# Performance work log

Hardware: AMD Instinct MI355X
Metric: run time of the kernel (lower is better)

The kernel has to match this reference:

```python
import jax, jax.numpy as jnp
import numpy as np

B, N, F = 16, 4096, 3

def setup_inputs() -> dict:
    key = jax.random.key(0)
    k1, k2 = jax.random.split(key)
    array1 = jax.random.normal(k1, (B, N, F), dtype=jnp.float32)
    array2 = jax.random.normal(k2, (B, N, F), dtype=jnp.float32)
    return {"array1": array1, "array2": array2}

def reference(array1, array2):
    # D[b, i, j] = ||array1[b, i] - array2[b, j]||^2, via expansion identity
    sq1 = jnp.sum(array1 * array1, axis=-1)              # [B, N1]
    sq2 = jnp.sum(array2 * array2, axis=-1)              # [B, N2]
    cross = jnp.einsum('bnd,bmd->bnm', array1, array2)   # [B, N1, N2]
    D = sq1[:, :, None] + sq2[:, None, :] - 2.0 * cross  # [B, N1, N2]
    # av_dist1: for each sample in array2, min dist to array1, then mean
    av_dist1 = jnp.mean(jnp.min(D, axis=1), axis=1)      # [B]
    # av_dist2: for each sample in array1, min dist to array2, then mean
    av_dist2 = jnp.mean(jnp.min(D, axis=2), axis=1)      # [B]
    dist = jnp.mean(0.5 * av_dist1 + 0.5 * av_dist2)
    return dist * 100.0
```

## Files before the change

### kernel.cpp

```cpp
#include <hip/hip_runtime.h>


constexpr int B_ = 16;
constexpr int N_ = 4096;
constexpr int BN = B_ * N_;
constexpr int BLK = 256;
constexpr int JTILES = N_ / 16;

using bf16x8 = __attribute__((ext_vector_type(8))) __bf16;
using f32x4  = __attribute__((ext_vector_type(4))) float;

__device__ inline uint bf16_rne(float f) {
    uint u = __float_as_uint(f);
    return (u + 0x7FFFu + ((u >> 16) & 1u)) >> 16;
}
__device__ inline float bf16_f(uint h) { return __uint_as_float(h << 16); }

__global__ __launch_bounds__(BLK)
void prep_kernel(const float* __restrict__ a1, const float* __restrict__ a2,
                 uint4* __restrict__ A1, uint4* __restrict__ B1,
                 uint4* __restrict__ A2, uint4* __restrict__ B2) {
    int gi = blockIdx.x * BLK + threadIdx.x;
    const float* in = blockIdx.y ? a2 : a1;
    uint4* Ao = blockIdx.y ? A2 : A1;
    uint4* Bo = blockIdx.y ? B2 : B1;
    float x = in[3 * gi], y = in[3 * gi + 1], z = in[3 * gi + 2];
    float sq = fmaf(x, x, fmaf(y, y, z * z));
    float t = -0.5f * sq;
    uint hx = bf16_rne(x), hy = bf16_rne(y), hz = bf16_rne(z);
    uint lx = bf16_rne(x - bf16_f(hx));
    uint ly = bf16_rne(y - bf16_f(hy));
    uint lz = bf16_rne(z - bf16_f(hz));
    uint th = bf16_rne(t);
    uint tl = bf16_rne(t - bf16_f(th));
    const uint ONE = 0x3F80u;
    Ao[2 * gi]     = make_uint4(hx | (hy << 16), hz | (lx << 16), ly | (lz << 16), hx | (hy << 16));
    Ao[2 * gi + 1] = make_uint4(hz | (ONE << 16), ONE | (th << 16), tl, 0u);
    Bo[2 * gi]     = make_uint4(hx | (hy << 16), hz | (hx << 16), hy | (hz << 16), lx | (ly << 16));
    Bo[2 * gi + 1] = make_uint4(lz | (th << 16), tl | (ONE << 16), ONE, 0u);
}

#define CSTEP(P_) {                                                            \
    f32x4 o0 = __builtin_amdgcn_mfma_f32_16x16x32_bf16(a0, (P_), cz, 0, 0, 0); \
    f32x4 o1 = __builtin_amdgcn_mfma_f32_16x16x32_bf16(a1, (P_), cz, 0, 0, 0); \
    vm0[0] = fmaxf(vm0[0], o0[0]); vm0[1] = fmaxf(vm0[1], o0[1]);              \
    vm0[2] = fmaxf(vm0[2], o0[2]); vm0[3] = fmaxf(vm0[3], o0[3]);              \
    vm1[0] = fmaxf(vm1[0], o1[0]); vm1[1] = fmaxf(vm1[1], o1[1]);              \
    vm1[2] = fmaxf(vm1[2], o1[2]); vm1[3] = fmaxf(vm1[3], o1[3]); }

__global__ __launch_bounds__(BLK, 4)
void minmax_kernel(const uint4* __restrict__ A1u, const uint4* __restrict__ B1u,
                   const uint4* __restrict__ A2u, const uint4* __restrict__ B2u,
                   float* __restrict__ vout) {
    int d = blockIdx.z, b = blockIdx.y;
    const bf16x8* __restrict__ Aarr = (const bf16x8*)(d ? A2u : A1u);
    const bf16x8* __restrict__ Barr = (const bf16x8*)(d ? B1u : B2u);
    int tid = threadIdx.x;
    int L = tid & 63, w = tid >> 6;
    int lpt = L & 15, hi = (L >> 4) & 1;
    bool act = L < 32;
    int ibase = blockIdx.x * 128 + w * 32;

    const bf16x8* pA = Aarr + (size_t)(b * N_ + ibase + lpt) * 2 + hi;
    const bf16x8* pB = Barr + (size_t)(b * N_ + lpt) * 2 + hi;

    uint4 zu; zu.x = zu.y = zu.z = zu.w = 0u;
    bf16x8 zf = __builtin_bit_cast(bf16x8, zu);
    bf16x8 a0 = act ? pA[0] : zf;
    bf16x8 a1 = act ? pA[32] : zf;
    f32x4 cz = {0.f, 0.f, 0.f, 0.f};
    f32x4 vm0 = {-3.0e38f, -3.0e38f, -3.0e38f, -3.0e38f};
    f32x4 vm1 = vm0;

    bf16x8 p0 = pB[0], p1 = pB[32], p2 = pB[64], p3 = pB[96];
#pragma unroll 1
    for (int jt = 0; jt < JTILES - 4; jt += 4) {
        bf16x8 n0 = pB[(size_t)(jt + 4) * 32], n1 = pB[(size_t)(jt + 5) * 32];
        bf16x8 n2 = pB[(size_t)(jt + 6) * 32], n3 = pB[(size_t)(jt + 7) * 32];
        CSTEP(p0) CSTEP(p1) CSTEP(p2) CSTEP(p3)
        p0 = n0; p1 = n1; p2 = n2; p3 = n3;
    }
    CSTEP(p0) CSTEP(p1) CSTEP(p2) CSTEP(p3)

#pragma unroll
    for (int off = 1; off < 16; off <<= 1) {
#pragma unroll
        for (int r = 0; r < 4; ++r) {
            vm0[r] = fmaxf(vm0[r], __shfl_xor(vm0[r], off));
            vm1[r] = fmaxf(vm1[r], __shfl_xor(vm1[r], off));
        }
    }
    if (lpt == 0) {
        int rg = L >> 4;
#pragma unroll
        for (int r = 0; r < 4; ++r) {
            int row = rg * 4 + r;
            int o = d * BN + b * N_ + ibase + row;
            vout[o] = -2.0f * vm0[r];
            vout[o + 16] = -2.0f * vm1[r];
        }
    }
}

__device__ inline float block_sum_256(float v, float* red4) {
    for (int off = 32; off; off >>= 1) v += __shfl_down(v, off, 64);
    int lane = threadIdx.x & 63, w = threadIdx.x >> 6;
    if (lane == 0) red4[w] = v;
    __syncthreads();
    return red4[0] + red4[1] + red4[2] + red4[3];
}

__global__ __launch_bounds__(BLK)
void reduce1_kernel(const float* __restrict__ vout, float* __restrict__ sums) {
    int t = blockIdx.x * BLK + threadIdx.x;
    float v = vout[t] + vout[BN + t];
    __shared__ float red4[4];
    float s = block_sum_256(v, red4);
    if (threadIdx.x == 0) sums[blockIdx.x] = s;
}

__global__ __launch_bounds__(BLK)
void reduce2_kernel(const float* __restrict__ sums, float* __restrict__ out) {
    float v = sums[threadIdx.x];
    __shared__ float red4[4];
    float s = block_sum_256(v, red4);
    if (threadIdx.x == 0) out[0] = s * (50.0f / (float)BN);
}

extern "C" void kernel_launch(void* const* d_in, const int* in_sizes, int n_in,
                              void* d_out, int out_size, void* d_ws, size_t ws_size,
                              hipStream_t stream) {
    const float* a1 = (const float*)d_in[0];
    const float* a2 = (const float*)d_in[1];
    char* ws = (char*)d_ws;
    uint4* A1 = (uint4*)(ws);
    uint4* B1 = (uint4*)(ws + (2u << 20));
    uint4* A2 = (uint4*)(ws + (4u << 20));
    uint4* B2 = (uint4*)(ws + (6u << 20));
    float* vout = (float*)(ws + (8u << 20));
    float* sums = (float*)(ws + (8u << 20) + (512u << 10));
    float* out = (float*)d_out;

    prep_kernel<<<dim3(BN / BLK, 2), BLK, 0, stream>>>(a1, a2, A1, B1, A2, B2);
    minmax_kernel<<<dim3(N_ / 128, B_, 2), BLK, 0, stream>>>(A1, B1, A2, B2, vout);
    reduce1_kernel<<<dim3(BN / BLK), BLK, 0, stream>>>(vout, sums);
    reduce2_kernel<<<dim3(1), BLK, 0, stream>>>(sums, out);
}
```

Before: 47.01 us.

## Split the j-dimension into two chunks to double minmax grid parallelism

The inner j loop of the min-distance kernel is split into two halves, each handled by a separate block (grid z goes from 2 to 4), and the partial maxima are combined in reduce1 before scaling. This is meant to raise occupancy and wave count on the many CUs, since the original grid had only 1024 blocks, each running a long serial loop. The prefetch depth also drops from 4 to 2 tiles, with paired MFMAs combined through a double fmax. The cost is double the A-operand loads, more vout traffic, and a shallower prefetch.

```diff
diff --git a/kernel.cpp b/kernel.cpp
--- a/kernel.cpp
+++ b/kernel.cpp
@@ -5,7 +5,9 @@
 constexpr int N_ = 4096;
 constexpr int BN = B_ * N_;
 constexpr int BLK = 256;
-constexpr int JTILES = N_ / 16;
+constexpr int JSPLIT = 2;
+constexpr int JCHUNK = N_ / JSPLIT;
+constexpr int JT = JCHUNK / 16;
 
 using bf16x8 = __attribute__((ext_vector_type(8))) __bf16;
 using f32x4  = __attribute__((ext_vector_type(4))) float;
@@ -40,19 +42,12 @@
     Bo[2 * gi + 1] = make_uint4(lz | (th << 16), tl | (ONE << 16), ONE, 0u);
 }
 
-#define CSTEP(P_) {                                                            \
-    f32x4 o0 = __builtin_amdgcn_mfma_f32_16x16x32_bf16(a0, (P_), cz, 0, 0, 0); \
-    f32x4 o1 = __builtin_amdgcn_mfma_f32_16x16x32_bf16(a1, (P_), cz, 0, 0, 0); \
-    vm0[0] = fmaxf(vm0[0], o0[0]); vm0[1] = fmaxf(vm0[1], o0[1]);              \
-    vm0[2] = fmaxf(vm0[2], o0[2]); vm0[3] = fmaxf(vm0[3], o0[3]);              \
-    vm1[0] = fmaxf(vm1[0], o1[0]); vm1[1] = fmaxf(vm1[1], o1[1]);              \
-    vm1[2] = fmaxf(vm1[2], o1[2]); vm1[3] = fmaxf(vm1[3], o1[3]); }
-
 __global__ __launch_bounds__(BLK, 4)
 void minmax_kernel(const uint4* __restrict__ A1u, const uint4* __restrict__ B1u,
                    const uint4* __restrict__ A2u, const uint4* __restrict__ B2u,
                    float* __restrict__ vout) {
-    int d = blockIdx.z, b = blockIdx.y;
+    int z = blockIdx.z, b = blockIdx.y;
+    int d = z >> 1, s = z & 1;
     const bf16x8* __restrict__ Aarr = (const bf16x8*)(d ? A2u : A1u);
     const bf16x8* __restrict__ Barr = (const bf16x8*)(d ? B1u : B2u);
     int tid = threadIdx.x;
@@ -62,7 +57,7 @@
     int ibase = blockIdx.x * 128 + w * 32;
 
     const bf16x8* pA = Aarr + (size_t)(b * N_ + ibase + lpt) * 2 + hi;
-    const bf16x8* pB = Barr + (size_t)(b * N_ + lpt) * 2 + hi;
+    const bf16x8* pB = Barr + (size_t)(b * N_ + s * JCHUNK + lpt) * 2 + hi;
 
     uint4 zu; zu.x = zu.y = zu.z = zu.w = 0u;
     bf16x8 zf = __builtin_bit_cast(bf16x8, zu);
@@ -72,15 +67,33 @@
     f32x4 vm0 = {-3.0e38f, -3.0e38f, -3.0e38f, -3.0e38f};
     f32x4 vm1 = vm0;
 
-    bf16x8 p0 = pB[0], p1 = pB[32], p2 = pB[64], p3 = pB[96];
+    bf16x8 q0 = pB[0], q1 = pB[32];
 #pragma unroll 1
-    for (int jt = 0; jt < JTILES - 4; jt += 4) {
-        bf16x8 n0 = pB[(size_t)(jt + 4) * 32], n1 = pB[(size_t)(jt + 5) * 32];
-        bf16x8 n2 = pB[(size_t)(jt + 6) * 32], n3 = pB[(size_t)(jt + 7) * 32];
-        CSTEP(p0) CSTEP(p1) CSTEP(p2) CSTEP(p3)
-        p0 = n0; p1 = n1; p2 = n2; p3 = n3;
+    for (int jt = 0; jt < JT - 2; jt += 2) {
+        bf16x8 n0 = pB[(size_t)(jt + 2) * 32];
+        bf16x8 n1 = pB[(size_t)(jt + 3) * 32];
+        f32x4 o0 = __builtin_amdgcn_mfma_f32_16x16x32_bf16(a0, q0, cz, 0, 0, 0);
+        f32x4 o1 = __builtin_amdgcn_mfma_f32_16x16x32_bf16(a1, q0, cz, 0, 0, 0);
+        f32x4 o2 = __builtin_amdgcn_mfma_f32_16x16x32_bf16(a0, q1, cz, 0, 0, 0);
+        f32x4 o3 = __builtin_amdgcn_mfma_f32_16x16x32_bf16(a1, q1, cz, 0, 0, 0);
+#pragma unroll
+        for (int r = 0; r < 4; ++r) {
+            vm0[r] = fmaxf(fmaxf(vm0[r], o0[r]), o2[r]);
+            vm1[r] = fmaxf(fmaxf(vm1[r], o1[r]), o3[r]);
+        }
+        q0 = n0; q1 = n1;
     }
-    CSTEP(p0) CSTEP(p1) CSTEP(p2) CSTEP(p3)
+    {
+        f32x4 o0 = __builtin_amdgcn_mfma_f32_16x16x32_bf16(a0, q0, cz, 0, 0, 0);
+        f32x4 o1 = __builtin_amdgcn_mfma_f32_16x16x32_bf16(a1, q0, cz, 0, 0, 0);
+        f32x4 o2 = __builtin_amdgcn_mfma_f32_16x16x32_bf16(a0, q1, cz, 0, 0, 0);
+        f32x4 o3 = __builtin_amdgcn_mfma_f32_16x16x32_bf16(a1, q1, cz, 0, 0, 0);
+#pragma unroll
+        for (int r = 0; r < 4; ++r) {
+            vm0[r] = fmaxf(fmaxf(vm0[r], o0[r]), o2[r]);
+            vm1[r] = fmaxf(fmaxf(vm1[r], o1[r]), o3[r]);
+        }
+    }
 
 #pragma unroll
     for (int off = 1; off < 16; off <<= 1) {
@@ -95,9 +108,9 @@
 #pragma unroll
         for (int r = 0; r < 4; ++r) {
             int row = rg * 4 + r;
-            int o = d * BN + b * N_ + ibase + row;
-            vout[o] = -2.0f * vm0[r];
-            vout[o + 16] = -2.0f * vm1[r];
+            int o = z * BN + b * N_ + ibase + row;
+            vout[o] = vm0[r];
+            vout[o + 16] = vm1[r];
         }
     }
 }
@@ -113,18 +126,20 @@
 __global__ __launch_bounds__(BLK)
 void reduce1_kernel(const float* __restrict__ vout, float* __restrict__ sums) {
     int t = blockIdx.x * BLK + threadIdx.x;
-    float v = vout[t] + vout[BN + t];
+    float m0 = fmaxf(vout[t], vout[BN + t]);
+    float m1 = fmaxf(vout[2 * BN + t], vout[3 * BN + t]);
+    float v = -2.0f * (m0 + m1);
     __shared__ float red4[4];
-    float s = block_sum_256(v, red4);
-    if (threadIdx.x == 0) sums[blockIdx.x] = s;
+    float sm = block_sum_256(v, red4);
+    if (threadIdx.x == 0) sums[blockIdx.x] = sm;
 }
 
 __global__ __launch_bounds__(BLK)
 void reduce2_kernel(const float* __restrict__ sums, float* __restrict__ out) {
     float v = sums[threadIdx.x];
     __shared__ float red4[4];
-    float s = block_sum_256(v, red4);
-    if (threadIdx.x == 0) out[0] = s * (50.0f / (float)BN);
+    float sm = block_sum_256(v, red4);
+    if (threadIdx.x == 0) out[0] = sm * (50.0f / (float)BN);
 }
 
 extern "C" void kernel_launch(void* const* d_in, const int* in_sizes, int n_in,
@@ -138,11 +153,11 @@
     uint4* A2 = (uint4*)(ws + (4u << 20));
     uint4* B2 = (uint4*)(ws + (6u << 20));
     float* vout = (float*)(ws + (8u << 20));
-    float* sums = (float*)(ws + (8u << 20) + (512u << 10));
+    float* sums = (float*)(ws + (9u << 20));
     float* out = (float*)d_out;
 
     prep_kernel<<<dim3(BN / BLK, 2), BLK, 0, stream>>>(a1, a2, A1, B1, A2, B2);
-    minmax_kernel<<<dim3(N_ / 128, B_, 2), BLK, 0, stream>>>(A1, B1, A2, B2, vout);
+    minmax_kernel<<<dim3(N_ / 128, B_, 2 * JSPLIT), BLK, 0, stream>>>(A1, B1, A2, B2, vout);
     reduce1_kernel<<<dim3(BN / BLK), BLK, 0, stream>>>(vout, sums);
     reduce2_kernel<<<dim3(1), BLK, 0, stream>>>(sums, out);
 }
```

After: 57.75 us. 22.8% more time.
